# Performance work log

Hardware: AMD Instinct MI355X
Metric: run time of the kernel (lower is better)

The kernel has to match this reference:

```python
import jax, jax.numpy as jnp
import numpy as np


def setup_inputs() -> dict:
    key = jax.random.key(0)
    k1, k2 = jax.random.split(key)
    # x: (B, C, D, H, W); w: (out_ch, C * 2*2*2)
    x = jax.random.normal(k1, (4, 64, 33, 33, 33), dtype=jnp.float32)
    w = jax.random.normal(k2, (128, 64 * 8), dtype=jnp.float32) * 0.05
    return {"x": x, "w": w}


def reference(x, w):
    # unfoldNd(kernel=2, stride=1, pad=0) + einsum('ij,kjm->kim', w, patches)
    # is exactly a valid 3D cross-correlation with a 2x2x2 kernel.
    B, C, D, H, W = x.shape
    O = w.shape[0]
    kern = w.reshape(O, C, 2, 2, 2)  # unfold flattening order: (C, kd, kh, kw)
    y = jax.lax.conv_general_dilated(
        x, kern,
        window_strides=(1, 1, 1),
        padding='VALID',
        dimension_numbers=('NCDHW', 'OIDHW', 'NCDHW'),
    )  # (B, O, D-1, H-1, W-1)
    return (y + 1.0) ** 2
```

## Files before the change

kernel.cpp:

```cpp
#include <hip/hip_runtime.h>

typedef __bf16 bf16x8 __attribute__((ext_vector_type(8)));
typedef float f32x4 __attribute__((ext_vector_type(4)));
typedef float f32x16 __attribute__((ext_vector_type(16)));
typedef unsigned short u16;
typedef unsigned int u32;
typedef u32 u32x4 __attribute__((ext_vector_type(4)));
typedef u16 u16x8 __attribute__((ext_vector_type(8)));

#define AS1 __attribute__((address_space(1)))
#define AS3 __attribute__((address_space(3)))
#define GLL16(gp, lp) __builtin_amdgcn_global_load_lds((const AS1 void*)(gp), (AS3 void*)(lp), 16, 0, 0)

__device__ __forceinline__ u16 f32_to_bf16_rne(float f) {
    union { float f; unsigned u; } cv; cv.f = f;
    unsigned u = cv.u;
    return (u16)((u + 0x7FFFu + ((u >> 16) & 1u)) >> 16);
}

__device__ __forceinline__ u32 cvt_pk_bf16(float lo, float hi) {
    u32 r;
    asm("v_cvt_pk_bf16_f32 %0, %1, %2" : "=v"(r) : "v"(lo), "v"(hi));
    return r;
}

__global__ __launch_bounds__(256) void prepass_kernel(
    const float* __restrict__ x, const float* __restrict__ w,
    u16* __restrict__ xT, u16* __restrict__ x32, u16* __restrict__ w4) {

    const int bid = blockIdx.x;
    const int tid = threadIdx.x;

    if (bid < 4356) {
        const int h = bid % 33;
        const int dq = bid / 33;
        const int d = dq % 33;
        const int b = dq / 33;
        const float* xp = x + (size_t)b * 2299968 + d * 1089 + h * 33;

        const int wv  = tid & 31;
        const int cc  = tid >> 5;
        const float* p = xp + (size_t)cc * 8 * 35937 + wv;
        float f0 = p[0],              f1 = p[35937],          f2 = p[2 * 35937], f3 = p[3 * 35937];
        float f4 = p[(size_t)4*35937],f5 = p[(size_t)5*35937],f6 = p[(size_t)6*35937],f7 = p[(size_t)7*35937];
        u32x4 v;
        v[0] = cvt_pk_bf16(f0, f1);
        v[1] = cvt_pk_bf16(f2, f3);
        v[2] = cvt_pk_bf16(f4, f5);
        v[3] = cvt_pk_bf16(f6, f7);
        *reinterpret_cast<u32x4*>(&xT[(size_t)bid * 2048 + cc * 256 + wv * 8]) = v;

        if (tid < 8) {
            const float* q = xp + (size_t)tid * 8 * 35937 + 32;
            u32x4 m;
            m[0] = cvt_pk_bf16(q[0],              q[35937]);
            m[1] = cvt_pk_bf16(q[2 * 35937],      q[3 * 35937]);
            m[2] = cvt_pk_bf16(q[(size_t)4*35937],q[(size_t)5*35937]);
            m[3] = cvt_pk_bf16(q[(size_t)6*35937],q[(size_t)7*35937]);
            *reinterpret_cast<u32x4*>(&x32[(size_t)bid * 64 + tid * 8]) = m;
        }
    } else {
        int e = (bid - 4356) * 256 + tid;
        int j    = e & 7;
        int half = (e >> 3) & 1;
        int o    = (e >> 4) & 127;
        int cq   = (e >> 11) & 3;
        int koff = (e >> 13) & 7;
        int c = cq * 16 + half * 8 + j;
        w4[e] = f32_to_bf16_rne(w[(o << 9) + (c << 3) + koff]);
    }
}

__global__ void repack_w_kernel(const float* __restrict__ w, u16* __restrict__ w3) {
    int e = blockIdx.x * 256 + threadIdx.x;
    int j    = e & 7;
    int g    = (e >> 3) & 3;
    int o    = (e >> 5) & 127;
    int cb   = (e >> 12) & 1;
    int koff = (e >> 13) & 7;
    int c = (cb << 5) + (g << 3) + j;
    w3[e] = f32_to_bf16_rne(w[(o << 9) + (c << 3) + koff]);
}

__global__ __launch_bounds__(256, 4) void conv_mfma_kernel(
    const u16* __restrict__ xT, const u16* __restrict__ x32,
    const u16* __restrict__ w4, float* __restrict__ out) {

    __shared__ __align__(16) u16 xs[12672];

    const int tid  = threadIdx.x;
    const int bid0 = blockIdx.x;
    const int wgid = ((bid0 & 7) << 8) + (bid0 >> 3);
    const int hyp  = wgid & 15;
    const int plane = wgid >> 4;
    const int dz   = plane & 31;
    const int b    = plane >> 5;
    const int hy0  = hyp << 1;

    char* ldsb = (char*)xs;
    const int slab0 = b * 1089 + dz * 33 + hy0;
#pragma unroll
    for (int r = 0; r < 6; ++r) {
        const int u   = tid + (r << 8);
        const int kd  = r >= 3;
        const int hh  = r - kd * 3;
        const char* src = (const char*)xT + ((size_t)(slab0 + kd * 33 + hh) << 12)
                          + ((u & 255) << 4);
        GLL16(src, ldsb + (u << 4));
    }
    if (tid < 48) {
        const int sid = tid >> 3;
        const int kd  = sid >= 3;
        const int hh  = sid - kd * 3;
        const char* src = (const char*)x32
            + ((size_t)(slab0 + kd * 33 + hh) << 7) + ((tid & 7) << 4);
        GLL16(src, ldsb + 24576 + (tid << 4));
    }
    asm volatile("s_waitcnt vmcnt(0)" ::: "memory");
    __syncthreads();

    const int lane = tid & 63;
    const int l31  = lane & 31;
    const int half = lane >> 5;
    const int o0   = (tid >> 6) << 5;

    f32x16 acc[2];
#pragma unroll
    for (int ht = 0; ht < 2; ++ht)
#pragma unroll
        for (int r = 0; r < 16; ++r)
            acc[ht][r] = 0.f;

#pragma unroll
    for (int kw = 0; kw < 2; ++kw) {
        const int row = l31 + kw;
#pragma unroll
        for (int cq = 0; cq < 4; ++cq) {
            const int cc = (cq << 1) + half;
            bf16x8 A[2][2];
#pragma unroll
            for (int kd = 0; kd < 2; ++kd)
#pragma unroll
                for (int kh = 0; kh < 2; ++kh) {
                    const int t = (((kd << 2) + (kh << 1) + kw) << 2) + cq;
                    const u16* p = w4 + (t << 11) + ((o0 + l31) << 4) + (half << 3);
                    A[kd][kh] = __builtin_bit_cast(bf16x8, *reinterpret_cast<const u16x8*>(p));
                }
            bf16x8 Bc[2], Bn[2];
#pragma unroll
            for (int kd = 0; kd < 2; ++kd) {
                const int sid = kd * 3;
                const u16* p = (row < 32)
                    ? &xs[(sid << 11) + (cc << 8) + (row << 3)]
                    : &xs[12288 + (sid << 6) + (cc << 3)];
                Bc[kd] = __builtin_bit_cast(bf16x8, *reinterpret_cast<const u16x8*>(p));
            }
#pragma unroll
            for (int ht = 0; ht < 2; ++ht) {
#pragma unroll
                for (int kd = 0; kd < 2; ++kd) {
                    const int sid = kd * 3 + ht + 1;
                    const u16* p = (row < 32)
                        ? &xs[(sid << 11) + (cc << 8) + (row << 3)]
                        : &xs[12288 + (sid << 6) + (cc << 3)];
                    Bn[kd] = __builtin_bit_cast(bf16x8, *reinterpret_cast<const u16x8*>(p));
                }
#pragma unroll
                for (int kd = 0; kd < 2; ++kd) {
                    acc[ht] = __builtin_amdgcn_mfma_f32_32x32x16_bf16(
                        A[kd][0], Bc[kd], acc[ht], 0, 0, 0);
                    acc[ht] = __builtin_amdgcn_mfma_f32_32x32x16_bf16(
                        A[kd][1], Bn[kd], acc[ht], 0, 0, 0);
                }
                Bc[0] = Bn[0];
                Bc[1] = Bn[1];
            }
        }
    }

    float* ob = out + (size_t)b * 128 * 32768 + ((size_t)dz << 10)
                + (hy0 << 5) + l31;
#pragma unroll
    for (int r = 0; r < 16; ++r) {
        const int orow = (r & 3) + ((r >> 2) << 3) + (half << 2);
        float* o2 = ob + ((size_t)(o0 + orow) << 15);
#pragma unroll
        for (int ht = 0; ht < 2; ++ht) {
            float v = acc[ht][r] + 1.0f;
            o2[ht << 5] = v * v;
        }
    }
}

#define XS_ROW 72
__global__ __launch_bounds__(256, 4) void conv_mfma_fallback(
    const float* __restrict__ x, const u16* __restrict__ w3, float* __restrict__ out) {

    __shared__ __align__(16) u16 xs[6 * 33 * XS_ROW];

    const int tid = threadIdx.x;
    const int bid = blockIdx.x;
    const int hy0 = (bid & 15) << 1;
    const int dz  = (bid >> 4) & 31;
    const int b   = bid >> 9;

    const float* xb = x + (size_t)b * 64 * 35937;
    for (int i = tid; i < 1584; i += 256) {
        int w   = i % 33;
        int t   = i / 33;
        int q   = t & 7;
        int kh3 = t >> 3;
        int kd  = kh3 >= 3 ? 1 : 0;
        int kh  = kh3 - kd * 3;
        const float* p = xb + (size_t)(q << 3) * 35937 + (dz + kd) * 1089 + (hy0 + kh) * 33 + w;
        u32x4 v;
        v[0] = cvt_pk_bf16(p[0], p[35937]);
        v[1] = cvt_pk_bf16(p[2 * 35937], p[3 * 35937]);
        v[2] = cvt_pk_bf16(p[4 * 35937], p[5 * 35937]);
        v[3] = cvt_pk_bf16(p[6 * 35937], p[7 * 35937]);
        *reinterpret_cast<u32x4*>(&xs[(kh3 * 33 + w) * XS_ROW + (q << 3)]) = v;
    }
    __syncthreads();

    const int lane = tid & 63;
    const int ln   = lane & 15;
    const int g    = lane >> 4;
    const int n0w  = (tid >> 6) << 5;

    f32x4 acc[2][4];
#pragma unroll
    for (int nf = 0; nf < 2; ++nf)
#pragma unroll
        for (int mf = 0; mf < 4; ++mf)
            acc[nf][mf] = (f32x4){0.f, 0.f, 0.f, 0.f};

#pragma unroll
    for (int cb = 0; cb < 2; ++cb) {
        const int cbase = (cb << 5) + (g << 3);
#pragma unroll
        for (int kd = 0; kd < 2; ++kd) {
            bf16x8 wf[2][4];
#pragma unroll
            for (int nf = 0; nf < 2; ++nf)
#pragma unroll
                for (int kk = 0; kk < 4; ++kk) {
                    const int koff = (kd << 2) + kk;
                    const u16* p = w3 + (size_t)((((koff << 1) + cb) << 7)
                                   + n0w + (nf << 4) + ln) * 32 + (g << 3);
                    wf[nf][kk] = __builtin_bit_cast(bf16x8, *reinterpret_cast<const u16x8*>(p));
                }
#pragma unroll
            for (int kw = 0; kw < 2; ++kw) {
                bf16x8 xf[3][2];
#pragma unroll
                for (int hh = 0; hh < 3; ++hh)
#pragma unroll
                    for (int wh = 0; wh < 2; ++wh) {
                        const int rw = (kd * 3 + hh) * 33 + (wh << 4) + ln + kw;
                        xf[hh][wh] = __builtin_bit_cast(bf16x8,
                            *reinterpret_cast<const u16x8*>(&xs[rw * XS_ROW + cbase]));
                    }
#pragma unroll
                for (int kh = 0; kh < 2; ++kh)
#pragma unroll
                    for (int nf = 0; nf < 2; ++nf)
#pragma unroll
                        for (int mf = 0; mf < 4; ++mf)
                            acc[nf][mf] = __builtin_amdgcn_mfma_f32_16x16x32_bf16(
                                wf[nf][(kh << 1) + kw], xf[(mf >> 1) + kh][mf & 1],
                                acc[nf][mf], 0, 0, 0);
            }
        }
    }

    float* ob = out + ((size_t)b * 128) * 32768 + (dz << 10) + (hy0 << 5);
#pragma unroll
    for (int nf = 0; nf < 2; ++nf)
#pragma unroll
        for (int mf = 0; mf < 4; ++mf) {
            const int wx   = ((mf & 1) << 4) + ln;
            const int hrow = mf >> 1;
            float* o2 = ob + (hrow << 5) + wx;
#pragma unroll
            for (int r = 0; r < 4; ++r) {
                const int n = n0w + (nf << 4) + (g << 2) + r;
                float v = acc[nf][mf][r] + 1.0f;
                o2[(size_t)n << 15] = v * v;
            }
        }
}

extern "C" void kernel_launch(void* const* d_in, const int* in_sizes, int n_in,
                              void* d_out, int out_size, void* d_ws, size_t ws_size,
                              hipStream_t stream) {
    const float* x = (const float*)d_in[0];
    const float* w = (const float*)d_in[1];
    float* out = (float*)d_out;

    const size_t W_BYTES   = 131072;
    const size_t XT_BYTES  = (size_t)4356 * 4096;
    const size_t X32_BYTES = (size_t)4356 * 128;
    const size_t NEED = W_BYTES + XT_BYTES + X32_BYTES;

    if (ws_size >= NEED) {
        u16* w4  = (u16*)d_ws;
        u16* xT  = (u16*)((char*)d_ws + W_BYTES);
        u16* x32 = (u16*)((char*)d_ws + W_BYTES + XT_BYTES);
        prepass_kernel<<<4612, 256, 0, stream>>>(x, w, xT, x32, w4);
        conv_mfma_kernel<<<2048, 256, 0, stream>>>(xT, x32, w4, out);
    } else {
        u16* w3 = (u16*)d_ws;
        repack_w_kernel<<<256, 256, 0, stream>>>(w, w3);
        conv_mfma_fallback<<<2048, 256, 0, stream>>>(x, w3, out);
    }
}
```

Before: 45.47 us.

## Make conv blocks process four h-tiles each with double-buffered async LDS staging

The MFMA conv kernel is split into stage and process helpers. Each workgroup now loops over four consecutive h-tile pairs, issuing global_load_lds for the next tile into a second LDS buffer while computing the current one, and the grid shrinks from 2048 to 512 blocks. The aim is to hide global-to-LDS latency behind MFMA work and amortize launch/prologue cost. In exchange, LDS per block doubles, fewer blocks are resident per CU, and correctness depends on hand-tuned vmcnt values that must match the exact count of outstanding memory operations.

```diff
diff --git a/kernel.cpp b/kernel.cpp
--- a/kernel.cpp
+++ b/kernel.cpp
@@ -82,42 +82,34 @@
     w3[e] = f32_to_bf16_rne(w[(o << 9) + (c << 3) + koff]);
 }
 
-__global__ __launch_bounds__(256, 4) void conv_mfma_kernel(
+__device__ __forceinline__ void stage_tile(
     const u16* __restrict__ xT, const u16* __restrict__ x32,
-    const u16* __restrict__ w4, float* __restrict__ out) {
-
-    __shared__ __align__(16) u16 xs[12672];
-
-    const int tid  = threadIdx.x;
-    const int bid0 = blockIdx.x;
-    const int wgid = ((bid0 & 7) << 8) + (bid0 >> 3);
-    const int hyp  = wgid & 15;
-    const int plane = wgid >> 4;
-    const int dz   = plane & 31;
-    const int b    = plane >> 5;
-    const int hy0  = hyp << 1;
-
-    char* ldsb = (char*)xs;
-    const int slab0 = b * 1089 + dz * 33 + hy0;
+    u16* __restrict__ buf, int slab0, int tid) {
+
+    char* ldsb = (char*)buf;
 #pragma unroll
     for (int r = 0; r < 6; ++r) {
-        const int u   = tid + (r << 8);
-        const int kd  = r >= 3;
-        const int hh  = r - kd * 3;
+        const int u  = tid + (r << 8);
+        const int kd = r >= 3;
+        const int hh = r - kd * 3;
         const char* src = (const char*)xT + ((size_t)(slab0 + kd * 33 + hh) << 12)
                           + ((u & 255) << 4);
         GLL16(src, ldsb + (u << 4));
     }
-    if (tid < 48) {
-        const int sid = tid >> 3;
+    const int l = tid & 63;
+    if (l < 48) {
+        const int sid = l >> 3;
         const int kd  = sid >= 3;
         const int hh  = sid - kd * 3;
         const char* src = (const char*)x32
-            + ((size_t)(slab0 + kd * 33 + hh) << 7) + ((tid & 7) << 4);
-        GLL16(src, ldsb + 24576 + (tid << 4));
-    }
-    asm volatile("s_waitcnt vmcnt(0)" ::: "memory");
-    __syncthreads();
+            + ((size_t)(slab0 + kd * 33 + hh) << 7) + ((l & 7) << 4);
+        GLL16(src, ldsb + 24576 + (l << 4));
+    }
+}
+
+__device__ __forceinline__ void process_tile(
+    const u16* __restrict__ buf, const u16* __restrict__ w4,
+    float* __restrict__ out, int b, int dz, int hy0, int tid) {
 
     const int lane = tid & 63;
     const int l31  = lane & 31;
@@ -151,8 +143,8 @@
             for (int kd = 0; kd < 2; ++kd) {
                 const int sid = kd * 3;
                 const u16* p = (row < 32)
-                    ? &xs[(sid << 11) + (cc << 8) + (row << 3)]
-                    : &xs[12288 + (sid << 6) + (cc << 3)];
+                    ? &buf[(sid << 11) + (cc << 8) + (row << 3)]
+                    : &buf[12288 + (sid << 6) + (cc << 3)];
                 Bc[kd] = __builtin_bit_cast(bf16x8, *reinterpret_cast<const u16x8*>(p));
             }
 #pragma unroll
@@ -161,8 +153,8 @@
                 for (int kd = 0; kd < 2; ++kd) {
                     const int sid = kd * 3 + ht + 1;
                     const u16* p = (row < 32)
-                        ? &xs[(sid << 11) + (cc << 8) + (row << 3)]
-                        : &xs[12288 + (sid << 6) + (cc << 3)];
+                        ? &buf[(sid << 11) + (cc << 8) + (row << 3)]
+                        : &buf[12288 + (sid << 6) + (cc << 3)];
                     Bn[kd] = __builtin_bit_cast(bf16x8, *reinterpret_cast<const u16x8*>(p));
                 }
 #pragma unroll
@@ -189,6 +181,41 @@
             float v = acc[ht][r] + 1.0f;
             o2[ht << 5] = v * v;
         }
+    }
+}
+
+__global__ __launch_bounds__(256, 4) void conv_mfma_kernel(
+    const u16* __restrict__ xT, const u16* __restrict__ x32,
+    const u16* __restrict__ w4, float* __restrict__ out) {
+
+    __shared__ __align__(16) u16 xs[2][12672];
+
+    const int tid  = threadIdx.x;
+    const int bid0 = blockIdx.x;
+    const int wgid = ((bid0 & 7) << 6) + (bid0 >> 3);
+    const int hq   = wgid & 3;
+    const int plane = wgid >> 2;
+    const int dz   = plane & 31;
+    const int b    = plane >> 5;
+    const int slabbase = b * 1089 + dz * 33;
+    const int hybase   = hq << 3;
+
+    stage_tile(xT, x32, xs[0], slabbase + hybase, tid);
+
+#pragma unroll
+    for (int t = 0; t < 4; ++t) {
+        if (t < 3)
+            stage_tile(xT, x32, xs[(t + 1) & 1], slabbase + hybase + ((t + 1) << 1), tid);
+
+        if (t == 0)      asm volatile("s_waitcnt vmcnt(7)"  ::: "memory");
+        else if (t == 3) asm volatile("s_waitcnt vmcnt(32)" ::: "memory");
+        else             asm volatile("s_waitcnt vmcnt(39)" ::: "memory");
+        __builtin_amdgcn_sched_barrier(0);
+        __builtin_amdgcn_s_barrier();
+
+        process_tile(xs[t & 1], w4, out, b, dz, hybase + (t << 1), tid);
+
+        __builtin_amdgcn_s_barrier();
     }
 }
 
@@ -307,7 +334,7 @@
         u16* xT  = (u16*)((char*)d_ws + W_BYTES);
         u16* x32 = (u16*)((char*)d_ws + W_BYTES + XT_BYTES);
         prepass_kernel<<<4612, 256, 0, stream>>>(x, w, xT, x32, w4);
-        conv_mfma_kernel<<<2048, 256, 0, stream>>>(xT, x32, w4, out);
+        conv_mfma_kernel<<<512, 256, 0, stream>>>(xT, x32, w4, out);
     } else {
         u16* w3 = (u16*)d_ws;
         repack_w_kernel<<<256, 256, 0, stream>>>(w, w3);
```

After: 45.71 us. No clear change (+0.5%).
